# Kernel optimization log

Measured on AMD Instinct MI355X. Metric: run time of the kernel, lower is better.

Reference implementation:

```python
import jax, jax.numpy as jnp
import numpy as np

B, C, H, W, D = 16, 512, 14, 14, 8000  # batch, channels(=input_dim1=input_dim2), spatial, output_dim


def _sketch_matrix(seed_h, seed_s, input_dim, output_dim):
    # Reproduce the module's count-sketch matrix generation (np.random.seed based).
    np.random.seed(seed_h)
    rand_h = np.random.randint(output_dim, size=input_dim)
    np.random.seed(seed_s)
    rand_s = (2 * np.random.randint(2, size=input_dim) - 1).astype(np.float32)
    M = np.zeros((input_dim, output_dim), dtype=np.float32)
    M[np.arange(input_dim), rand_h] = rand_s  # one-hot-per-row with sign
    return jnp.asarray(M)


def setup_inputs() -> dict:
    key = jax.random.key(0)
    x = jax.random.normal(key, (B, C, H, W), dtype=jnp.float32)
    S1 = _sketch_matrix(1, 3, C, D)
    S2 = _sketch_matrix(5, 7, C, D)
    return {"x": x, "S1": S1, "S2": S2}


def reference(x, S1, S2):
    b, c, h, w = x.shape
    # NCHW -> (B*H*W, C)
    flat = jnp.transpose(x, (0, 2, 3, 1)).reshape(-1, c)
    sketch1 = flat @ S1  # [BHW, D]
    sketch2 = flat @ S2  # [BHW, D]
    # circular convolution of the two count-sketches via FFT
    f1 = jnp.fft.fft(sketch1, axis=-1)
    f2 = jnp.fft.fft(sketch2, axis=-1)
    cbp_flat = jnp.fft.ifft(f1 * f2, axis=-1).real.astype(x.dtype)
    cbp = cbp_flat.reshape(b, h, w, -1)
    # sum_pool=True: reduce over spatial dims -> [B, D]
    return cbp.sum(axis=(1, 2))
```

## Files before the change

kernel.cpp:

```cpp
#include <hip/hip_runtime.h>

#define B_DIM 16
#define C_DIM 512
#define HW_DIM 196
#define D_DIM 8000
#define KP 224
#define NROW (B_DIM * C_DIM)

typedef __attribute__((ext_vector_type(8))) short short8;
typedef __attribute__((ext_vector_type(4))) float float4v;

__global__ __launch_bounds__(256) void prep(
    const float* __restrict__ x, const float* __restrict__ S1,
    const float* __restrict__ S2,
    int* __restrict__ h, float* __restrict__ s,
    unsigned short* __restrict__ xp, float* __restrict__ out) {
    const int bid = blockIdx.x;
    const int tid = threadIdx.x;
    if (bid < 2 * C_DIM) {
        const int row   = bid & (C_DIM - 1);
        const int which = bid >> 9;
        const float4* rowp = (const float4*)((which ? S2 : S1) + (size_t)row * D_DIM);
        int*   hp = h + which * C_DIM;
        float* sp = s + which * C_DIM;
        for (int j4 = tid; j4 < D_DIM / 4; j4 += 256) {
            float4 v = rowp[j4];
            if (v.x != 0.0f) { hp[row] = 4 * j4 + 0; sp[row] = v.x; }
            if (v.y != 0.0f) { hp[row] = 4 * j4 + 1; sp[row] = v.y; }
            if (v.z != 0.0f) { hp[row] = 4 * j4 + 2; sp[row] = v.z; }
            if (v.w != 0.0f) { hp[row] = 4 * j4 + 3; sp[row] = v.w; }
        }
    } else {
        const int j = bid - 2 * C_DIM;
        #pragma unroll
        for (int l = 0; l < 14; ++l) {
            int idx = l * 256 + tid;
            int r   = idx / KP;
            int kk  = idx - r * KP;
            int row = j * 16 + r;
            float v = (kk < HW_DIM) ? x[(size_t)row * HW_DIM + kk] : 0.0f;
            unsigned int u = __float_as_uint(v);
            u = (u + 0x7FFFu + ((u >> 16) & 1u)) >> 16;
            xp[(size_t)row * KP + kk] = (unsigned short)u;
        }
        if (j < 500) out[j * 256 + tid] = 0.0f;
    }
}

__global__ __launch_bounds__(256) void gram_hist(
    const unsigned short* __restrict__ xp,
    const int* __restrict__ h1, const float* __restrict__ s1,
    const int* __restrict__ h2, const float* __restrict__ s2,
    float* __restrict__ out) {
    const int b  = blockIdx.z;
    const int i0 = blockIdx.y * 128;
    const int j0 = blockIdx.x * 64;

    __shared__ float hist[D_DIM];
    const int tid = threadIdx.x;
    for (int d = tid; d < D_DIM; d += 256) hist[d] = 0.0f;
    __syncthreads();

    const int w  = tid >> 6;
    const int l  = tid & 63;
    const int rA = l & 15;
    const int g  = l >> 4;

    const unsigned short* base = xp + (size_t)b * C_DIM * KP;
    const unsigned short* pA[2];
    const unsigned short* pB[4];
    #pragma unroll
    for (int mt = 0; mt < 2; ++mt)
        pA[mt] = base + (size_t)(i0 + w * 32 + mt * 16 + rA) * KP + g * 8;
    #pragma unroll
    for (int nt = 0; nt < 4; ++nt)
        pB[nt] = base + (size_t)(j0 + nt * 16 + rA) * KP + g * 8;

    float4v acc[2][4];
    #pragma unroll
    for (int mt = 0; mt < 2; ++mt)
        #pragma unroll
        for (int nt = 0; nt < 4; ++nt)
            acc[mt][nt] = (float4v){0.0f, 0.0f, 0.0f, 0.0f};

    short8 fa[2], fb[4];
    #pragma unroll
    for (int mt = 0; mt < 2; ++mt) fa[mt] = *(const short8*)pA[mt];
    #pragma unroll
    for (int nt = 0; nt < 4; ++nt) fb[nt] = *(const short8*)pB[nt];

    #pragma unroll
    for (int step = 1; step <= 7; ++step) {
        short8 na[2], nb[4];
        if (step < 7) {
            #pragma unroll
            for (int mt = 0; mt < 2; ++mt) na[mt] = *(const short8*)(pA[mt] + step * 32);
            #pragma unroll
            for (int nt = 0; nt < 4; ++nt) nb[nt] = *(const short8*)(pB[nt] + step * 32);
        }
        #pragma unroll
        for (int mt = 0; mt < 2; ++mt)
            #pragma unroll
            for (int nt = 0; nt < 4; ++nt)
                acc[mt][nt] = __builtin_amdgcn_mfma_f32_16x16x32_bf16(
                    fa[mt], fb[nt], acc[mt][nt], 0, 0, 0);
        if (step < 7) {
            #pragma unroll
            for (int mt = 0; mt < 2; ++mt) fa[mt] = na[mt];
            #pragma unroll
            for (int nt = 0; nt < 4; ++nt) fb[nt] = nb[nt];
        }
    }

    int hr[2][4]; float sr[2][4]; int hc[4]; float sc[4];
    #pragma unroll
    for (int mt = 0; mt < 2; ++mt)
        #pragma unroll
        for (int r = 0; r < 4; ++r) {
            int c1 = i0 + w * 32 + mt * 16 + (l >> 4) * 4 + r;
            hr[mt][r] = h1[c1]; sr[mt][r] = s1[c1];
        }
    #pragma unroll
    for (int nt = 0; nt < 4; ++nt) {
        int c2 = j0 + nt * 16 + (l & 15);
        hc[nt] = h2[c2]; sc[nt] = s2[c2];
    }
    #pragma unroll
    for (int mt = 0; mt < 2; ++mt)
        #pragma unroll
        for (int nt = 0; nt < 4; ++nt)
            #pragma unroll
            for (int r = 0; r < 4; ++r) {
                int bin = hr[mt][r] + hc[nt];
                if (bin >= D_DIM) bin -= D_DIM;
                atomicAdd(&hist[bin], sr[mt][r] * sc[nt] * acc[mt][nt][r]);
            }
    __syncthreads();

    float* outb = out + (size_t)b * D_DIM;
    for (int d = tid; d < D_DIM; d += 256) {
        float v = hist[d];
        if (v != 0.0f) atomicAdd(outb + d, v);
    }
}

extern "C" void kernel_launch(void* const* d_in, const int* in_sizes, int n_in,
                              void* d_out, int out_size, void* d_ws, size_t ws_size,
                              hipStream_t stream) {
    const float* x  = (const float*)d_in[0];
    const float* S1 = (const float*)d_in[1];
    const float* S2 = (const float*)d_in[2];
    float* out = (float*)d_out;

    int*            h  = (int*)d_ws;
    float*          s  = (float*)(h + 2 * C_DIM);
    unsigned short* xp = (unsigned short*)(s + 2 * C_DIM);

    prep<<<2 * C_DIM + NROW / 16, 256, 0, stream>>>(x, S1, S2, h, s, xp, out);

    dim3 grid(C_DIM / 64, C_DIM / 128, B_DIM);
    gram_hist<<<grid, 256, 0, stream>>>(xp, h, s, h + C_DIM, s + C_DIM, out);
}
```

Measured before the change: 122.4 us.

## Replace global atomic histogram flush with per-block partials and a reduction kernel

Each gram_hist block now writes its full shared-memory histogram to a private partial buffer with vectorized stores, replacing the sparse global atomicAdds into the output. A new reduce_part kernel sums the 32 partials per batch, so the output no longer has to be zeroed in prep. The aim is to remove atomic contention on global memory. In exchange it writes about 16 MB of partials, reads them back, and adds a third kernel launch. Shared histogram zeroing is also vectorized to float4.

Result: faster. 117.5 us (-4.0%).

```diff
diff --git a/kernel.cpp b/kernel.cpp
--- a/kernel.cpp
+++ b/kernel.cpp
@@ -6,6 +6,7 @@
 #define D_DIM 8000
 #define KP 224
 #define NROW (B_DIM * C_DIM)
+#define NBLK 512
 
 typedef __attribute__((ext_vector_type(8))) short short8;
 typedef __attribute__((ext_vector_type(4))) float float4v;
@@ -14,7 +15,7 @@
     const float* __restrict__ x, const float* __restrict__ S1,
     const float* __restrict__ S2,
     int* __restrict__ h, float* __restrict__ s,
-    unsigned short* __restrict__ xp, float* __restrict__ out) {
+    unsigned short* __restrict__ xp) {
     const int bid = blockIdx.x;
     const int tid = threadIdx.x;
     if (bid < 2 * C_DIM) {
@@ -43,7 +44,6 @@
             u = (u + 0x7FFFu + ((u >> 16) & 1u)) >> 16;
             xp[(size_t)row * KP + kk] = (unsigned short)u;
         }
-        if (j < 500) out[j * 256 + tid] = 0.0f;
     }
 }
 
@@ -51,14 +51,18 @@
     const unsigned short* __restrict__ xp,
     const int* __restrict__ h1, const float* __restrict__ s1,
     const int* __restrict__ h2, const float* __restrict__ s2,
-    float* __restrict__ out) {
+    float* __restrict__ part) {
     const int b  = blockIdx.z;
     const int i0 = blockIdx.y * 128;
     const int j0 = blockIdx.x * 64;
 
-    __shared__ float hist[D_DIM];
+    __shared__ __align__(16) float hist[D_DIM];
     const int tid = threadIdx.x;
-    for (int d = tid; d < D_DIM; d += 256) hist[d] = 0.0f;
+    #pragma unroll
+    for (int l = 0; l < D_DIM / 1024; ++l)
+        ((float4*)hist)[l * 256 + tid] = (float4){0.f, 0.f, 0.f, 0.f};
+    if (tid < D_DIM / 4 - (D_DIM / 1024) * 256)
+        ((float4*)hist)[(D_DIM / 1024) * 256 + tid] = (float4){0.f, 0.f, 0.f, 0.f};
     __syncthreads();
 
     const int w  = tid >> 6;
@@ -137,11 +141,26 @@
             }
     __syncthreads();
 
-    float* outb = out + (size_t)b * D_DIM;
-    for (int d = tid; d < D_DIM; d += 256) {
-        float v = hist[d];
-        if (v != 0.0f) atomicAdd(outb + d, v);
-    }
+    float* pb = part + (size_t)(((size_t)b * 4 + blockIdx.y) * 8 + blockIdx.x) * D_DIM;
+    #pragma unroll
+    for (int l4 = 0; l4 < D_DIM / 1024; ++l4)
+        ((float4*)pb)[l4 * 256 + tid] = ((const float4*)hist)[l4 * 256 + tid];
+    if (tid < D_DIM / 4 - (D_DIM / 1024) * 256)
+        ((float4*)pb)[(D_DIM / 1024) * 256 + tid] =
+            ((const float4*)hist)[(D_DIM / 1024) * 256 + tid];
+}
+
+__global__ __launch_bounds__(256) void reduce_part(
+    const float* __restrict__ part, float* __restrict__ out) {
+    int idx = blockIdx.x * 256 + threadIdx.x;
+    if (idx >= B_DIM * D_DIM) return;
+    int b = idx / D_DIM;
+    int d = idx - b * D_DIM;
+    const float* p = part + (size_t)b * 32 * D_DIM + d;
+    float v = 0.0f;
+    #pragma unroll
+    for (int t = 0; t < 32; ++t) v += p[(size_t)t * D_DIM];
+    out[idx] = v;
 }
 
 extern "C" void kernel_launch(void* const* d_in, const int* in_sizes, int n_in,
@@ -152,12 +171,15 @@
     const float* S2 = (const float*)d_in[2];
     float* out = (float*)d_out;
 
-    int*            h  = (int*)d_ws;
-    float*          s  = (float*)(h + 2 * C_DIM);
-    unsigned short* xp = (unsigned short*)(s + 2 * C_DIM);
+    int*            h    = (int*)d_ws;
+    float*          s    = (float*)(h + 2 * C_DIM);
+    unsigned short* xp   = (unsigned short*)(s + 2 * C_DIM);
+    float*          part = (float*)(xp + (size_t)NROW * KP);
 
-    prep<<<2 * C_DIM + NROW / 16, 256, 0, stream>>>(x, S1, S2, h, s, xp, out);
+    prep<<<2 * C_DIM + NROW / 16, 256, 0, stream>>>(x, S1, S2, h, s, xp);
 
     dim3 grid(C_DIM / 64, C_DIM / 128, B_DIM);
-    gram_hist<<<grid, 256, 0, stream>>>(xp, h, s, h + C_DIM, s + C_DIM, out);
+    gram_hist<<<grid, 256, 0, stream>>>(xp, h, s, h + C_DIM, s + C_DIM, part);
+
+    reduce_part<<<(B_DIM * D_DIM + 255) / 256, 256, 0, stream>>>(part, out);
 }
```

## Replace global atomics with per-block partials and last-block reduction; widen N tile

Applied to the files above, without the earlier changes.

Each gram_hist block now covers a 128x128 tile instead of 128x64 and writes its full shared histogram to a partial buffer. A per-batch counter elects the last finishing block, which sums the 16 partials into the output, replacing global atomicAdds and the separate zeroing of out. The sketch-matrix scan now handles two rows per block and exits early once the nonzero entry is found. In exchange the kernel adds a partial-buffer round trip, a threadfence-based counter protocol and higher register pressure.

Result: slower. 129.4 us (+5.7%).

```diff
diff --git a/kernel.cpp b/kernel.cpp
--- a/kernel.cpp
+++ b/kernel.cpp
@@ -14,24 +14,37 @@
     const float* __restrict__ x, const float* __restrict__ S1,
     const float* __restrict__ S2,
     int* __restrict__ h, float* __restrict__ s,
-    unsigned short* __restrict__ xp, float* __restrict__ out) {
+    unsigned short* __restrict__ xp, unsigned int* __restrict__ cnt) {
     const int bid = blockIdx.x;
     const int tid = threadIdx.x;
-    if (bid < 2 * C_DIM) {
-        const int row   = bid & (C_DIM - 1);
-        const int which = bid >> 9;
-        const float4* rowp = (const float4*)((which ? S2 : S1) + (size_t)row * D_DIM);
-        int*   hp = h + which * C_DIM;
-        float* sp = s + which * C_DIM;
-        for (int j4 = tid; j4 < D_DIM / 4; j4 += 256) {
-            float4 v = rowp[j4];
-            if (v.x != 0.0f) { hp[row] = 4 * j4 + 0; sp[row] = v.x; }
-            if (v.y != 0.0f) { hp[row] = 4 * j4 + 1; sp[row] = v.y; }
-            if (v.z != 0.0f) { hp[row] = 4 * j4 + 2; sp[row] = v.z; }
-            if (v.w != 0.0f) { hp[row] = 4 * j4 + 3; sp[row] = v.w; }
+    if (bid < 2 * C_DIM / 2) {
+        __shared__ int found;
+        for (int rr = 0; rr < 2; ++rr) {
+            const int r     = bid * 2 + rr;
+            const int row   = r & (C_DIM - 1);
+            const int which = r >> 9;
+            const float4* rowp = (const float4*)((which ? S2 : S1) + (size_t)row * D_DIM);
+            int*   hp = h + which * C_DIM;
+            float* sp = s + which * C_DIM;
+            if (tid == 0) found = 0;
+            __syncthreads();
+            for (int c = 0; c < 8; ++c) {
+                int j4 = c * 256 + tid;
+                if (j4 < D_DIM / 4) {
+                    float4 v = rowp[j4];
+                    if (v.x != 0.f) { hp[row] = 4 * j4 + 0; sp[row] = v.x; found = 1; }
+                    if (v.y != 0.f) { hp[row] = 4 * j4 + 1; sp[row] = v.y; found = 1; }
+                    if (v.z != 0.f) { hp[row] = 4 * j4 + 2; sp[row] = v.z; found = 1; }
+                    if (v.w != 0.f) { hp[row] = 4 * j4 + 3; sp[row] = v.w; found = 1; }
+                }
+                __syncthreads();
+                if (found) break;
+            }
+            __syncthreads();
         }
     } else {
-        const int j = bid - 2 * C_DIM;
+        const int j = bid - 512;
+        if (j == 0 && tid < B_DIM) cnt[tid] = 0;
         #pragma unroll
         for (int l = 0; l < 14; ++l) {
             int idx = l * 256 + tid;
@@ -43,22 +56,30 @@
             u = (u + 0x7FFFu + ((u >> 16) & 1u)) >> 16;
             xp[(size_t)row * KP + kk] = (unsigned short)u;
         }
-        if (j < 500) out[j * 256 + tid] = 0.0f;
     }
 }
 
-__global__ __launch_bounds__(256) void gram_hist(
+__global__ __launch_bounds__(256, 1) void gram_hist(
     const unsigned short* __restrict__ xp,
-    const int* __restrict__ h1, const float* __restrict__ s1,
-    const int* __restrict__ h2, const float* __restrict__ s2,
+    const int* __restrict__ h, const float* __restrict__ s,
+    float* __restrict__ part,
+    unsigned int* __restrict__ cnt,
     float* __restrict__ out) {
+    const int jb = blockIdx.x;
+    const int ib = blockIdx.y;
     const int b  = blockIdx.z;
-    const int i0 = blockIdx.y * 128;
-    const int j0 = blockIdx.x * 64;
-
-    __shared__ float hist[D_DIM];
+    const int i0 = ib * 128;
+    const int j0 = jb * 128;
     const int tid = threadIdx.x;
-    for (int d = tid; d < D_DIM; d += 256) hist[d] = 0.0f;
+
+    __shared__ __align__(16) float hist[D_DIM];
+    __shared__ int lastFlag;
+
+    #pragma unroll
+    for (int l4 = 0; l4 < 7; ++l4)
+        ((float4*)hist)[l4 * 256 + tid] = (float4){0.f, 0.f, 0.f, 0.f};
+    if (tid < 2000 - 1792)
+        ((float4*)hist)[1792 + tid] = (float4){0.f, 0.f, 0.f, 0.f};
     __syncthreads();
 
     const int w  = tid >> 6;
@@ -68,79 +89,103 @@
 
     const unsigned short* base = xp + (size_t)b * C_DIM * KP;
     const unsigned short* pA[2];
-    const unsigned short* pB[4];
+    const unsigned short* pB[8];
     #pragma unroll
     for (int mt = 0; mt < 2; ++mt)
         pA[mt] = base + (size_t)(i0 + w * 32 + mt * 16 + rA) * KP + g * 8;
     #pragma unroll
-    for (int nt = 0; nt < 4; ++nt)
+    for (int nt = 0; nt < 8; ++nt)
         pB[nt] = base + (size_t)(j0 + nt * 16 + rA) * KP + g * 8;
 
-    float4v acc[2][4];
-    #pragma unroll
-    for (int mt = 0; mt < 2; ++mt)
-        #pragma unroll
-        for (int nt = 0; nt < 4; ++nt)
+    float4v acc[2][8];
+    #pragma unroll
+    for (int mt = 0; mt < 2; ++mt)
+        #pragma unroll
+        for (int nt = 0; nt < 8; ++nt)
             acc[mt][nt] = (float4v){0.0f, 0.0f, 0.0f, 0.0f};
 
-    short8 fa[2], fb[4];
+    short8 fa[2], fb[8];
     #pragma unroll
     for (int mt = 0; mt < 2; ++mt) fa[mt] = *(const short8*)pA[mt];
     #pragma unroll
-    for (int nt = 0; nt < 4; ++nt) fb[nt] = *(const short8*)pB[nt];
+    for (int nt = 0; nt < 8; ++nt) fb[nt] = *(const short8*)pB[nt];
 
     #pragma unroll
     for (int step = 1; step <= 7; ++step) {
-        short8 na[2], nb[4];
+        short8 na[2], nb[8];
         if (step < 7) {
             #pragma unroll
             for (int mt = 0; mt < 2; ++mt) na[mt] = *(const short8*)(pA[mt] + step * 32);
             #pragma unroll
-            for (int nt = 0; nt < 4; ++nt) nb[nt] = *(const short8*)(pB[nt] + step * 32);
+            for (int nt = 0; nt < 8; ++nt) nb[nt] = *(const short8*)(pB[nt] + step * 32);
         }
         #pragma unroll
         for (int mt = 0; mt < 2; ++mt)
             #pragma unroll
-            for (int nt = 0; nt < 4; ++nt)
+            for (int nt = 0; nt < 8; ++nt)
                 acc[mt][nt] = __builtin_amdgcn_mfma_f32_16x16x32_bf16(
                     fa[mt], fb[nt], acc[mt][nt], 0, 0, 0);
         if (step < 7) {
             #pragma unroll
             for (int mt = 0; mt < 2; ++mt) fa[mt] = na[mt];
             #pragma unroll
-            for (int nt = 0; nt < 4; ++nt) fb[nt] = nb[nt];
-        }
-    }
-
-    int hr[2][4]; float sr[2][4]; int hc[4]; float sc[4];
-    #pragma unroll
-    for (int mt = 0; mt < 2; ++mt)
-        #pragma unroll
-        for (int r = 0; r < 4; ++r) {
-            int c1 = i0 + w * 32 + mt * 16 + (l >> 4) * 4 + r;
-            hr[mt][r] = h1[c1]; sr[mt][r] = s1[c1];
-        }
-    #pragma unroll
-    for (int nt = 0; nt < 4; ++nt) {
+            for (int nt = 0; nt < 8; ++nt) fb[nt] = nb[nt];
+        }
+    }
+
+    int hr[2][4]; float sr[2][4]; int hc[8]; float sc[8];
+    #pragma unroll
+    for (int mt = 0; mt < 2; ++mt)
+        #pragma unroll
+        for (int rg = 0; rg < 4; ++rg) {
+            int c1 = i0 + w * 32 + mt * 16 + (l >> 4) * 4 + rg;
+            hr[mt][rg] = h[c1]; sr[mt][rg] = s[c1];
+        }
+    #pragma unroll
+    for (int nt = 0; nt < 8; ++nt) {
         int c2 = j0 + nt * 16 + (l & 15);
-        hc[nt] = h2[c2]; sc[nt] = s2[c2];
-    }
-    #pragma unroll
-    for (int mt = 0; mt < 2; ++mt)
-        #pragma unroll
-        for (int nt = 0; nt < 4; ++nt)
-            #pragma unroll
-            for (int r = 0; r < 4; ++r) {
-                int bin = hr[mt][r] + hc[nt];
+        hc[nt] = h[C_DIM + c2]; sc[nt] = s[C_DIM + c2];
+    }
+    #pragma unroll
+    for (int mt = 0; mt < 2; ++mt)
+        #pragma unroll
+        for (int nt = 0; nt < 8; ++nt)
+            #pragma unroll
+            for (int rg = 0; rg < 4; ++rg) {
+                int bin = hr[mt][rg] + hc[nt];
                 if (bin >= D_DIM) bin -= D_DIM;
-                atomicAdd(&hist[bin], sr[mt][r] * sc[nt] * acc[mt][nt][r]);
+                atomicAdd(&hist[bin], sr[mt][rg] * sc[nt] * acc[mt][nt][rg]);
             }
     __syncthreads();
 
-    float* outb = out + (size_t)b * D_DIM;
-    for (int d = tid; d < D_DIM; d += 256) {
-        float v = hist[d];
-        if (v != 0.0f) atomicAdd(outb + d, v);
+    const int slot = (b * 4 + ib) * 4 + jb;
+    float* pb = part + (size_t)slot * D_DIM;
+    #pragma unroll
+    for (int l4 = 0; l4 < 7; ++l4)
+        ((float4*)pb)[l4 * 256 + tid] = ((const float4*)hist)[l4 * 256 + tid];
+    if (tid < 2000 - 1792)
+        ((float4*)pb)[1792 + tid] = ((const float4*)hist)[1792 + tid];
+    __syncthreads();
+
+    if (tid == 0) {
+        __threadfence();
+        unsigned int old = atomicAdd(&cnt[b], 1u);
+        lastFlag = (old == 15u);
+    }
+    __syncthreads();
+    if (lastFlag) {
+        __threadfence();
+        const float4* pp = (const float4*)(part + (size_t)b * 16 * D_DIM);
+        float4* ob = (float4*)(out + (size_t)b * D_DIM);
+        for (int i4 = tid; i4 < D_DIM / 4; i4 += 256) {
+            float4 v = {0.f, 0.f, 0.f, 0.f};
+            #pragma unroll
+            for (int t = 0; t < 16; ++t) {
+                float4 p = pp[(size_t)t * (D_DIM / 4) + i4];
+                v.x += p.x; v.y += p.y; v.z += p.z; v.w += p.w;
+            }
+            ob[i4] = v;
+        }
     }
 }
 
@@ -152,12 +197,14 @@
     const float* S2 = (const float*)d_in[2];
     float* out = (float*)d_out;
 
-    int*            h  = (int*)d_ws;
-    float*          s  = (float*)(h + 2 * C_DIM);
-    unsigned short* xp = (unsigned short*)(s + 2 * C_DIM);
-
-    prep<<<2 * C_DIM + NROW / 16, 256, 0, stream>>>(x, S1, S2, h, s, xp, out);
-
-    dim3 grid(C_DIM / 64, C_DIM / 128, B_DIM);
-    gram_hist<<<grid, 256, 0, stream>>>(xp, h, s, h + C_DIM, s + C_DIM, out);
+    int*            h    = (int*)d_ws;
+    float*          s    = (float*)(h + 2 * C_DIM);
+    unsigned short* xp   = (unsigned short*)(s + 2 * C_DIM);
+    float*          part = (float*)(xp + (size_t)NROW * KP);
+    unsigned int*   cnt  = (unsigned int*)(part + 256 * D_DIM);
+
+    prep<<<1024, 256, 0, stream>>>(x, S1, S2, h, s, xp, cnt);
+
+    dim3 grid(4, 4, B_DIM);
+    gram_hist<<<grid, 256, 0, stream>>>(xp, h, s, part, cnt, out);
 }
```
